# Kernel tuning notes

Measured on AMD Instinct MI355X. Metric: run time of the kernel, lower is better.

Reference implementation:

```python
import jax, jax.numpy as jnp
import numpy as np

ALPHA = 0.2          # LeakyReLU negative slope
NEG_INF = -9e15      # mask value from the torch code
B, N, F, E, H, S, T, L = 32, 128, 78, 12, 256, 20, 13, 3


def setup_inputs() -> dict:
    key = jax.random.key(0)
    ks = jax.random.split(key, 20)
    sc = 0.05  # param scale
    inp = {
        "node_features": jax.random.normal(ks[0], (B, N, F), jnp.float32),
        "edge_features": jax.random.normal(ks[1], (B, N, N, E), jnp.float32),
        "adj_matrix": jax.random.randint(ks[2], (B, N, N), 0, 2).astype(jnp.int32),
        "scaffold_features": jax.random.normal(ks[3], (B, S), jnp.float32),
        # node projection (Linear F->H, with bias)
        "W_node": jax.random.normal(ks[4], (F, H), jnp.float32) * sc,
        "b_node": jnp.zeros((H,), jnp.float32),
        # stacked GAT layer params: W (H->H, no bias), a (2H->1, no bias)
        "gat_W": jax.random.normal(ks[5], (L, H, H), jnp.float32) * sc,
        "gat_a": jax.random.normal(ks[6], (L, 2 * H), jnp.float32) * sc,
        # scaffold projection (S->H)
        "W_sc": jax.random.normal(ks[7], (S, H), jnp.float32) * sc,
        "b_sc": jnp.zeros((H,), jnp.float32),
        # graph_pooling MLP: H -> H/2 -> H/4 (shared for graph + scaffold paths)
        "gp_w1": jax.random.normal(ks[8], (H, H // 2), jnp.float32) * sc,
        "gp_b1": jnp.zeros((H // 2,), jnp.float32),
        "gp_w2": jax.random.normal(ks[9], (H // 2, H // 4), jnp.float32) * sc,
        "gp_b2": jnp.zeros((H // 4,), jnp.float32),
        # output MLP: (H/4 + H/4) -> H/2 -> T
        "out_w1": jax.random.normal(ks[10], (H // 2, H // 2), jnp.float32) * sc,
        "out_b1": jnp.zeros((H // 2,), jnp.float32),
        "out_w2": jax.random.normal(ks[11], (H // 2, T), jnp.float32) * sc,
        "out_b2": jnp.zeros((T,), jnp.float32),
    }
    return inp


def _gat_stack(x, adj_matrix, gat_W, gat_a):
    # x: (B,N,H); adj: (B,N,N) int
    mask = adj_matrix > 0
    n_layers, _, h_dim = gat_W.shape
    for l in range(n_layers):
        h = jnp.einsum("bnf,fh->bnh", x, gat_W[l])      # (B,N,H)
        a1, a2 = gat_a[l, :h_dim], gat_a[l, h_dim:]
        # a . [h_i ; h_j] == h_i.a1 + h_j.a2 (exact decomposition of the
        # O(N^2, 2H) concat in the torch code)
        s1 = h @ a1                                       # (B,N)
        s2 = h @ a2                                       # (B,N)
        e = jax.nn.leaky_relu(s1[:, :, None] + s2[:, None, :], ALPHA)
        att = jnp.where(mask, e, NEG_INF)                 # (B,N,N)
        att = jax.nn.softmax(att, axis=-1)
        h_prime = jnp.einsum("bij,bjh->bih", att, h)
        x = jax.nn.relu(h_prime)                          # relu after layer (dropout = identity, eval)
    return x


def _pool(z, gp_w1, gp_b1, gp_w2, gp_b2):
    z = jax.nn.relu(z @ gp_w1 + gp_b1)
    return jax.nn.relu(z @ gp_w2 + gp_b2)


def reference(node_features, edge_features, adj_matrix, scaffold_features,
              W_node, b_node, gat_W, gat_a, W_sc, b_sc,
              gp_w1, gp_b1, gp_w2, gp_b2, out_w1, out_b1, out_w2, out_b2):
    # edge_features is accepted but unused in the original forward
    x = node_features @ W_node + b_node                  # (B,N,H)
    x = _gat_stack(x, adj_matrix, gat_W, gat_a)
    graph = x.mean(axis=1)                               # (B,H)
    g = _pool(graph, gp_w1, gp_b1, gp_w2, gp_b2)         # (B,H/4)
    s = _pool(scaffold_features @ W_sc + b_sc, gp_w1, gp_b1, gp_w2, gp_b2)
    c = jnp.concatenate([g, s], axis=-1)                 # (B,H/2)
    hdn = jax.nn.relu(c @ out_w1 + out_b1)
    return hdn @ out_w2 + out_b2                         # (B,T)
```

## Files before the change

### kernel.cpp

```cpp
#include <hip/hip_runtime.h>
#include <hip/hip_bf16.h>

#define NEG_INF -9.0e15f

using u16 = unsigned short;

__device__ __forceinline__ float b2f(__hip_bfloat16 v) { return __bfloat162float(v); }
__device__ __forceinline__ float ldv(const float* p, int i) { return p[i]; }
__device__ __forceinline__ float ldv(const __hip_bfloat16* p, int i) { return __bfloat162float(p[i]); }

__device__ __forceinline__ void async16(const void* g, void* l) {
    __builtin_amdgcn_global_load_lds(
        (__attribute__((address_space(1))) void*)(g),
        (__attribute__((address_space(3))) void*)(l), 16, 0, 0);
}

__device__ __forceinline__ int sniff(const void* wnode) {
    const u16* w = (const u16*)wnode;
    int lane = threadIdx.x & 63;
    u16 u = w[2 * lane];
    int e = (u >> 7) & 0xFF;
    unsigned long long m = __ballot(e >= 100 && e <= 140);
    return __popcll(m) >= 48;
}

__global__ __launch_bounds__(256) void k_rep(
    const void* __restrict__ gat_W, const void* __restrict__ W_node,
    u16* __restrict__ Wrep, u16* __restrict__ Wnrep) {
    if (!sniff(W_node)) return;
    int b = blockIdx.x, t = threadIdx.x;
    if (b < 384) {
        int c = b / 48, idx = (b % 48) * 256 + t;
        ((uint4*)(Wrep + (size_t)c * 196608))[idx] = ((const uint4*)gat_W)[idx];
    } else {
        int bb = b - 384;
        int c = bb / 5, idx = (bb % 5) * 256 + t;
        if (idx < 1248)
            ((uint4*)(Wnrep + (size_t)c * 19968))[idx] = ((const uint4*)W_node)[idx];
    }
}

__global__ __launch_bounds__(256) void k_gat(
    const float* __restrict__ x, const void* __restrict__ gat_W,
    const u16* __restrict__ Wrep, const void* __restrict__ gat_a, int layer,
    const void* __restrict__ nf, const void* __restrict__ Wn_raw,
    const u16* __restrict__ Wnrep, const void* __restrict__ bn, int first,
    float* __restrict__ h, float* __restrict__ s1, float* __restrict__ s2) {
    __shared__ float xsT[256 * 10];
    const int t = threadIdx.x;
    const int bx = blockIdx.x;
    const int row0 = bx * 8;
    const int tx = t & 63, w = t >> 6;
    const int isbf = sniff(Wn_raw);
    const int c0 = 4 * tx;

    float acc0[4], acc1[4];

    if (isbf) {
        if (first) {
            const u16* nfu = (const u16*)nf;
            for (int i = t; i < 624; i += 256) {
                int r = i / 78, k = i - r * 78;
                xsT[k * 10 + r] = __uint_as_float(((unsigned)nfu[(row0 + r) * 78 + k]) << 16);
            }
            __syncthreads();
            const u16* Wnl = Wnrep + (size_t)(bx & 7) * 19968;
            const __hip_bfloat16* bnb = (const __hip_bfloat16*)bn;
            #pragma unroll
            for (int j = 0; j < 4; ++j) { acc0[j] = b2f(bnb[c0 + j]); acc1[j] = acc0[j]; }
            #pragma unroll 2
            for (int k = 0; k < 78; ++k) {
                uint2 wv = *(const uint2*)(Wnl + k * 256 + c0);
                float w0 = __uint_as_float(wv.x << 16);
                float w1 = __uint_as_float(wv.x & 0xffff0000u);
                float w2 = __uint_as_float(wv.y << 16);
                float w3 = __uint_as_float(wv.y & 0xffff0000u);
                float2 xp = *(const float2*)&xsT[k * 10 + 2 * w];
                acc0[0] += xp.x * w0; acc0[1] += xp.x * w1;
                acc0[2] += xp.x * w2; acc0[3] += xp.x * w3;
                acc1[0] += xp.y * w0; acc1[1] += xp.y * w1;
                acc1[2] += xp.y * w2; acc1[3] += xp.y * w3;
            }
            __syncthreads();
            #pragma unroll
            for (int j = 0; j < 4; ++j) {
                xsT[(c0 + j) * 10 + 2 * w]     = acc0[j];
                xsT[(c0 + j) * 10 + 2 * w + 1] = acc1[j];
            }
            __syncthreads();
        } else {
            int r = t >> 5, cb = (t & 31) * 8;
            const float4* xp = (const float4*)(x + (size_t)(row0 + r) * 256 + cb);
            float4 f0 = xp[0], f1 = xp[1];
            xsT[(cb + 0) * 10 + r] = f0.x; xsT[(cb + 1) * 10 + r] = f0.y;
            xsT[(cb + 2) * 10 + r] = f0.z; xsT[(cb + 3) * 10 + r] = f0.w;
            xsT[(cb + 4) * 10 + r] = f1.x; xsT[(cb + 5) * 10 + r] = f1.y;
            xsT[(cb + 6) * 10 + r] = f1.z; xsT[(cb + 7) * 10 + r] = f1.w;
            __syncthreads();
        }
        const u16* Wl = Wrep + (size_t)(bx & 7) * 196608 + (size_t)layer * 65536;
        #pragma unroll
        for (int j = 0; j < 4; ++j) { acc0[j] = 0.f; acc1[j] = 0.f; }
        #pragma unroll 4
        for (int k = 0; k < 256; ++k) {
            uint2 wv = *(const uint2*)(Wl + k * 256 + c0);
            float w0 = __uint_as_float(wv.x << 16);
            float w1 = __uint_as_float(wv.x & 0xffff0000u);
            float w2 = __uint_as_float(wv.y << 16);
            float w3 = __uint_as_float(wv.y & 0xffff0000u);
            float2 xp = *(const float2*)&xsT[k * 10 + 2 * w];
            acc0[0] += xp.x * w0; acc0[1] += xp.x * w1;
            acc0[2] += xp.x * w2; acc0[3] += xp.x * w3;
            acc1[0] += xp.y * w0; acc1[1] += xp.y * w1;
            acc1[2] += xp.y * w2; acc1[3] += xp.y * w3;
        }
        const __hip_bfloat16* ga = (const __hip_bfloat16*)gat_a + (size_t)layer * 512;
        float d10 = 0.f, d20 = 0.f, d11 = 0.f, d21 = 0.f;
        #pragma unroll
        for (int j = 0; j < 4; ++j) {
            float a1v = b2f(ga[c0 + j]), a2v = b2f(ga[256 + c0 + j]);
            d10 += acc0[j] * a1v; d20 += acc0[j] * a2v;
            d11 += acc1[j] * a1v; d21 += acc1[j] * a2v;
        }
        #pragma unroll
        for (int off = 1; off < 64; off <<= 1) {
            d10 += __shfl_xor(d10, off, 64); d20 += __shfl_xor(d20, off, 64);
            d11 += __shfl_xor(d11, off, 64); d21 += __shfl_xor(d21, off, 64);
        }
        if (tx == 0) {
            s1[row0 + 2 * w] = d10;     s2[row0 + 2 * w] = d20;
            s1[row0 + 2 * w + 1] = d11; s2[row0 + 2 * w + 1] = d21;
        }
        *(float4*)&h[(size_t)(row0 + 2 * w) * 256 + c0]     = (float4){acc0[0], acc0[1], acc0[2], acc0[3]};
        *(float4*)&h[(size_t)(row0 + 2 * w + 1) * 256 + c0] = (float4){acc1[0], acc1[1], acc1[2], acc1[3]};
    } else {
        const float* Wlf = (const float*)gat_W + (size_t)layer * 65536;
        const float* gaf = (const float*)gat_a + (size_t)layer * 512;
        if (first) {
            const float* nff = (const float*)nf;
            for (int i = t; i < 624; i += 256) {
                int r = i / 78, k = i - r * 78;
                xsT[k * 10 + r] = nff[(row0 + r) * 78 + k];
            }
            __syncthreads();
            const float* Wnf = (const float*)Wn_raw;
            const float* bnf = (const float*)bn;
            #pragma unroll
            for (int j = 0; j < 4; ++j) { acc0[j] = bnf[c0 + j]; acc1[j] = acc0[j]; }
            for (int k = 0; k < 78; ++k) {
                float4 wf = *(const float4*)(Wnf + k * 256 + c0);
                float2 xp = *(const float2*)&xsT[k * 10 + 2 * w];
                acc0[0] += xp.x * wf.x; acc0[1] += xp.x * wf.y;
                acc0[2] += xp.x * wf.z; acc0[3] += xp.x * wf.w;
                acc1[0] += xp.y * wf.x; acc1[1] += xp.y * wf.y;
                acc1[2] += xp.y * wf.z; acc1[3] += xp.y * wf.w;
            }
            __syncthreads();
            #pragma unroll
            for (int j = 0; j < 4; ++j) {
                xsT[(c0 + j) * 10 + 2 * w]     = acc0[j];
                xsT[(c0 + j) * 10 + 2 * w + 1] = acc1[j];
            }
            __syncthreads();
        } else {
            int r = t >> 5, cb = (t & 31) * 8;
            const float4* xp = (const float4*)(x + (size_t)(row0 + r) * 256 + cb);
            float4 f0 = xp[0], f1 = xp[1];
            xsT[(cb + 0) * 10 + r] = f0.x; xsT[(cb + 1) * 10 + r] = f0.y;
            xsT[(cb + 2) * 10 + r] = f0.z; xsT[(cb + 3) * 10 + r] = f0.w;
            xsT[(cb + 4) * 10 + r] = f1.x; xsT[(cb + 5) * 10 + r] = f1.y;
            xsT[(cb + 6) * 10 + r] = f1.z; xsT[(cb + 7) * 10 + r] = f1.w;
            __syncthreads();
        }
        #pragma unroll
        for (int j = 0; j < 4; ++j) { acc0[j] = 0.f; acc1[j] = 0.f; }
        #pragma unroll 4
        for (int k = 0; k < 256; ++k) {
            float4 wf = *(const float4*)(Wlf + k * 256 + c0);
            float2 xp = *(const float2*)&xsT[k * 10 + 2 * w];
            acc0[0] += xp.x * wf.x; acc0[1] += xp.x * wf.y;
            acc0[2] += xp.x * wf.z; acc0[3] += xp.x * wf.w;
            acc1[0] += xp.y * wf.x; acc1[1] += xp.y * wf.y;
            acc1[2] += xp.y * wf.z; acc1[3] += xp.y * wf.w;
        }
        float d10 = 0.f, d20 = 0.f, d11 = 0.f, d21 = 0.f;
        #pragma unroll
        for (int j = 0; j < 4; ++j) {
            float a1v = gaf[c0 + j], a2v = gaf[256 + c0 + j];
            d10 += acc0[j] * a1v; d20 += acc0[j] * a2v;
            d11 += acc1[j] * a1v; d21 += acc1[j] * a2v;
        }
        #pragma unroll
        for (int off = 1; off < 64; off <<= 1) {
            d10 += __shfl_xor(d10, off, 64); d20 += __shfl_xor(d20, off, 64);
            d11 += __shfl_xor(d11, off, 64); d21 += __shfl_xor(d21, off, 64);
        }
        if (tx == 0) {
            s1[row0 + 2 * w] = d10;     s2[row0 + 2 * w] = d20;
            s1[row0 + 2 * w + 1] = d11; s2[row0 + 2 * w + 1] = d21;
        }
        *(float4*)&h[(size_t)(row0 + 2 * w) * 256 + c0]     = (float4){acc0[0], acc0[1], acc0[2], acc0[3]};
        *(float4*)&h[(size_t)(row0 + 2 * w + 1) * 256 + c0] = (float4){acc1[0], acc1[1], acc1[2], acc1[3]};
    }
}

__global__ __launch_bounds__(256) void k_attn(
    const float* __restrict__ h, const float* __restrict__ s1,
    const float* __restrict__ s2, const int* __restrict__ adj,
    float* __restrict__ x, float* __restrict__ gpart, int do_pool) {
    __shared__ float att_t[128][10];
    __shared__ __align__(16) float hbuf[2][32 * 256];
    __shared__ float pool_red[4][256];
    int blk = blockIdx.x, b = blk >> 4, i0 = (blk & 15) << 3;
    int t = threadIdx.x, w = t >> 6, lane = t & 63;
    const char* hbytes = (const char*)(h + (size_t)b * 32768);
    const int ph = blk & 3;
    {
        char* lb = (char*)&hbuf[0][0];
        const char* g = hbytes + ph * 32768;
        #pragma unroll
        for (int i = 0; i < 8; ++i)
            async16(g + i * 4096 + t * 16, lb + i * 4096 + t * 16);
    }
    {
        int cc0 = lane, cc1 = lane + 64;
        int ir0 = i0 + 2 * w, ir1 = ir0 + 1;
        const int* a0 = adj + (size_t)(b * 128 + ir0) * 128;
        const int* a1 = adj + (size_t)(b * 128 + ir1) * 128;
        int m00 = a0[cc0], m01 = a0[cc1], m10 = a1[cc0], m11 = a1[cc1];
        float sv0 = s1[b * 128 + ir0], sv1 = s1[b * 128 + ir1];
        float t0 = s2[b * 128 + cc0],  t1 = s2[b * 128 + cc1];
        float e00 = sv0 + t0; e00 = (e00 >= 0.f) ? e00 : 0.2f * e00;
        float e01 = sv0 + t1; e01 = (e01 >= 0.f) ? e01 : 0.2f * e01;
        float e10 = sv1 + t0; e10 = (e10 >= 0.f) ? e10 : 0.2f * e10;
        float e11 = sv1 + t1; e11 = (e11 >= 0.f) ? e11 : 0.2f * e11;
        float v00 = (m00 > 0) ? e00 : NEG_INF;
        float v01 = (m01 > 0) ? e01 : NEG_INF;
        float v10 = (m10 > 0) ? e10 : NEG_INF;
        float v11 = (m11 > 0) ? e11 : NEG_INF;
        float mx0 = fmaxf(v00, v01), mx1 = fmaxf(v10, v11);
        #pragma unroll
        for (int off = 1; off < 64; off <<= 1) {
            mx0 = fmaxf(mx0, __shfl_xor(mx0, off, 64));
            mx1 = fmaxf(mx1, __shfl_xor(mx1, off, 64));
        }
        float p00 = __expf(v00 - mx0), p01 = __expf(v01 - mx0);
        float p10 = __expf(v10 - mx1), p11 = __expf(v11 - mx1);
        float s0 = p00 + p01, ss1 = p10 + p11;
        #pragma unroll
        for (int off = 1; off < 64; off <<= 1) {
            s0  += __shfl_xor(s0, off, 64);
            ss1 += __shfl_xor(ss1, off, 64);
        }
        float inv0 = 1.0f / s0, inv1 = 1.0f / ss1;
        att_t[cc0][2 * w]     = p00 * inv0;
        att_t[cc1][2 * w]     = p01 * inv0;
        att_t[cc0][2 * w + 1] = p10 * inv1;
        att_t[cc1][2 * w + 1] = p11 * inv1;
    }
    __syncthreads();
    int tx = t & 63, ty = t >> 6;
    float acc0[4] = {0.f, 0.f, 0.f, 0.f}, acc1[4] = {0.f, 0.f, 0.f, 0.f};
    for (int c = 0; c < 4; ++c) {
        if (c < 3) {
            char* lb = (char*)&hbuf[(c + 1) & 1][0];
            const char* g = hbytes + (((c + 1 + ph) & 3) * 32768);
            #pragma unroll
            for (int i = 0; i < 8; ++i)
                async16(g + i * 4096 + t * 16, lb + i * 4096 + t * 16);
        }
        const float* hc = &hbuf[c & 1][0];
        const int jb = ((c + ph) & 3) * 32;
        #pragma unroll 4
        for (int jj = 0; jj < 32; ++jj) {
            float4 hv = *(const float4*)&hc[jj * 256 + 4 * tx];
            float2 ap = *(const float2*)&att_t[jb + jj][2 * ty];
            acc0[0] += ap.x * hv.x; acc0[1] += ap.x * hv.y;
            acc0[2] += ap.x * hv.z; acc0[3] += ap.x * hv.w;
            acc1[0] += ap.y * hv.x; acc1[1] += ap.y * hv.y;
            acc1[2] += ap.y * hv.z; acc1[3] += ap.y * hv.w;
        }
        __syncthreads();
    }
    if (!do_pool) {
        float4 o0 = {fmaxf(acc0[0],0.f), fmaxf(acc0[1],0.f), fmaxf(acc0[2],0.f), fmaxf(acc0[3],0.f)};
        float4 o1 = {fmaxf(acc1[0],0.f), fmaxf(acc1[1],0.f), fmaxf(acc1[2],0.f), fmaxf(acc1[3],0.f)};
        *(float4*)&x[(size_t)(b * 128 + i0 + 2 * ty)     * 256 + 4 * tx] = o0;
        *(float4*)&x[(size_t)(b * 128 + i0 + 2 * ty + 1) * 256 + 4 * tx] = o1;
    } else {
        float4 pr = {(fmaxf(acc0[0],0.f) + fmaxf(acc1[0],0.f)) * (1.f/128.f),
                     (fmaxf(acc0[1],0.f) + fmaxf(acc1[1],0.f)) * (1.f/128.f),
                     (fmaxf(acc0[2],0.f) + fmaxf(acc1[2],0.f)) * (1.f/128.f),
                     (fmaxf(acc0[3],0.f) + fmaxf(acc1[3],0.f)) * (1.f/128.f)};
        *(float4*)&pool_red[ty][4 * tx] = pr;
        __syncthreads();
        if (t < 64) {
            float4 r0 = ((const float4*)&pool_red[0][0])[t];
            float4 r1 = ((const float4*)&pool_red[1][0])[t];
            float4 r2 = ((const float4*)&pool_red[2][0])[t];
            float4 r3 = ((const float4*)&pool_red[3][0])[t];
            float4 o = {r0.x+r1.x+r2.x+r3.x, r0.y+r1.y+r2.y+r3.y,
                        r0.z+r1.z+r2.z+r3.z, r0.w+r1.w+r2.w+r3.w};
            *(float4*)&gpart[((size_t)b * 16 + (blk & 15)) * 256 + 4 * t] = o;
        }
    }
}

template <typename T>
__device__ __forceinline__ void head_body(
    int b, int t, const float* __restrict__ gpart,
    const T* scaf, const T* W_sc, const T* b_sc,
    const T* gp_w1, const T* gp_b1, const T* gp_w2, const T* gp_b2,
    const T* out_w1, const T* out_b1, const T* out_w2, const T* out_b2,
    float* gin_s, float* sproj, float* scaf_s,
    float* red1, float* red2, float* z1g, float* z1s,
    float* cvec, float* hdn, float* outv) {
    float g = 0.f;
    #pragma unroll
    for (int gg = 0; gg < 16; ++gg) g += gpart[((size_t)b * 16 + gg) * 256 + t];
    gin_s[t] = g;
    if (t < 20) scaf_s[t] = ldv(scaf, b * 20 + t);
    __syncthreads();
    {
        float sa = ldv(b_sc, t);
        #pragma unroll
        for (int k = 0; k < 20; ++k) sa += scaf_s[k] * ldv(W_sc, k * 256 + t);
        sproj[t] = sa;
    }
    __syncthreads();
    {
        int j = t & 127, khalf = t >> 7;
        int k0 = khalf * 128;
        float a1 = 0.f, a2 = 0.f;
        #pragma unroll 16
        for (int kk = 0; kk < 128; ++kk) {
            int k = k0 + kk;
            float wv = ldv(gp_w1, k * 128 + j);
            a1 += gin_s[k] * wv;
            a2 += sproj[k] * wv;
        }
        red1[t] = a1; red2[t] = a2;
    }
    __syncthreads();
    if (t < 128) {
        float bb = ldv(gp_b1, t);
        z1g[t] = fmaxf(bb + red1[t] + red1[t + 128], 0.f);
        z1s[t] = fmaxf(bb + red2[t] + red2[t + 128], 0.f);
    }
    __syncthreads();
    {
        int j = t & 63, q = t >> 6;
        int k0 = q * 32;
        float a1 = 0.f, a2 = 0.f;
        #pragma unroll
        for (int kk = 0; kk < 32; ++kk) {
            int k = k0 + kk;
            float wv = ldv(gp_w2, k * 64 + j);
            a1 += z1g[k] * wv;
            a2 += z1s[k] * wv;
        }
        red1[t] = a1; red2[t] = a2;
    }
    __syncthreads();
    if (t < 64) {
        float bb = ldv(gp_b2, t);
        cvec[t]      = fmaxf(bb + red1[t] + red1[t + 64] + red1[t + 128] + red1[t + 192], 0.f);
        cvec[64 + t] = fmaxf(bb + red2[t] + red2[t + 64] + red2[t + 128] + red2[t + 192], 0.f);
    }
    __syncthreads();
    {
        int j = t & 127, khalf = t >> 7;
        int k0 = khalf * 64;
        float a = 0.f;
        #pragma unroll 16
        for (int kk = 0; kk < 64; ++kk) {
            int k = k0 + kk;
            a += cvec[k] * ldv(out_w1, k * 128 + j);
        }
        red1[t] = a;
    }
    __syncthreads();
    if (t < 128) hdn[t] = fmaxf(ldv(out_b1, t) + red1[t] + red1[t + 128], 0.f);
    __syncthreads();
    if (t < 13) {
        float a = ldv(out_b2, t);
        #pragma unroll 16
        for (int k = 0; k < 128; ++k) a += hdn[k] * ldv(out_w2, k * 13 + t);
        outv[t] = a;
    }
}

__global__ __launch_bounds__(256) void k_head(
    const float* __restrict__ gpart, const void* __restrict__ scaf,
    const void* __restrict__ W_sc, const void* __restrict__ b_sc,
    const void* __restrict__ gp_w1, const void* __restrict__ gp_b1,
    const void* __restrict__ gp_w2, const void* __restrict__ gp_b2,
    const void* __restrict__ out_w1, const void* __restrict__ out_b1,
    const void* __restrict__ out_w2, const void* __restrict__ out_b2,
    void* __restrict__ out, const void* __restrict__ Wn) {
    int isbf = sniff(Wn);
    int b = blockIdx.x;
    int t = threadIdx.x;
    __shared__ float gin_s[256], sproj[256], scaf_s[20];
    __shared__ float red1[256], red2[256];
    __shared__ float z1g[128], z1s[128], cvec[128], hdn[128], outv[13];
    if (isbf) {
        head_body<__hip_bfloat16>(b, t, gpart,
            (const __hip_bfloat16*)scaf, (const __hip_bfloat16*)W_sc, (const __hip_bfloat16*)b_sc,
            (const __hip_bfloat16*)gp_w1, (const __hip_bfloat16*)gp_b1,
            (const __hip_bfloat16*)gp_w2, (const __hip_bfloat16*)gp_b2,
            (const __hip_bfloat16*)out_w1, (const __hip_bfloat16*)out_b1,
            (const __hip_bfloat16*)out_w2, (const __hip_bfloat16*)out_b2,
            gin_s, sproj, scaf_s, red1, red2, z1g, z1s, cvec, hdn, outv);
    } else {
        head_body<float>(b, t, gpart,
            (const float*)scaf, (const float*)W_sc, (const float*)b_sc,
            (const float*)gp_w1, (const float*)gp_b1,
            (const float*)gp_w2, (const float*)gp_b2,
            (const float*)out_w1, (const float*)out_b1,
            (const float*)out_w2, (const float*)out_b2,
            gin_s, sproj, scaf_s, red1, red2, z1g, z1s, cvec, hdn, outv);
    }
    __syncthreads();
    if (t < 13) {
        if (isbf) ((__hip_bfloat16*)out)[b * 13 + t] = __float2bfloat16(outv[t]);
        else      ((float*)out)[b * 13 + t] = outv[t];
    }
}

extern "C" void kernel_launch(void* const* d_in, const int* in_sizes, int n_in,
                              void* d_out, int out_size, void* d_ws, size_t ws_size,
                              hipStream_t stream) {
    (void)in_sizes; (void)n_in; (void)out_size; (void)ws_size;
    const void* nf     = d_in[0];
    const int*  adj    = (const int*)d_in[2];
    const void* scaf   = d_in[3];
    const void* W_node = d_in[4];
    const void* b_node = d_in[5];
    const void* gat_W  = d_in[6];
    const void* gat_a  = d_in[7];
    const void* W_sc   = d_in[8];
    const void* b_sc   = d_in[9];
    const void* gp_w1  = d_in[10];
    const void* gp_b1  = d_in[11];
    const void* gp_w2  = d_in[12];
    const void* gp_b2  = d_in[13];
    const void* out_w1 = d_in[14];
    const void* out_b1 = d_in[15];
    const void* out_w2 = d_in[16];
    const void* out_b2 = d_in[17];

    float* ws    = (float*)d_ws;
    float* x     = ws;
    float* h     = ws + 1048576;
    float* s1    = ws + 2097152;
    float* s2    = s1 + 4096;
    float* gpart = s2 + 4096;
    u16*   Wrep  = (u16*)(gpart + 131072);
    u16*   Wnrep = Wrep + 8 * 196608;

    k_rep<<<424, 256, 0, stream>>>(gat_W, W_node, Wrep, Wnrep);
    for (int l = 0; l < 3; ++l) {
        k_gat<<<512, 256, 0, stream>>>(x, gat_W, Wrep, gat_a, l,
                                       nf, W_node, Wnrep, b_node, (l == 0) ? 1 : 0,
                                       h, s1, s2);
        k_attn<<<512, 256, 0, stream>>>(h, s1, s2, adj, x, gpart, (l == 2) ? 1 : 0);
    }
    k_head<<<32, 256, 0, stream>>>(gpart, scaf, W_sc, b_sc, gp_w1, gp_b1, gp_w2, gp_b2,
                                   out_w1, out_b1, out_w2, out_b2, d_out, W_node);
}
```

Measured before the change: 227.2 us.

## Drop weight replication kernel and halve rows per GAT projection block

Removes the k_rep kernel that copied gat_W and W_node into eight per-XCD replicas, so k_gat now reads the original weights directly. Each k_gat block now handles 4 rows (one per wave) instead of 8, and the grid doubles to 1024 blocks. The x tile is stored untransposed in shared memory. This saves one launch and the replication traffic and adds parallelism, at the cost of halving weight reuse per block and possible L2 contention across XCDs on the shared weights.

```diff
diff --git a/kernel.cpp b/kernel.cpp
--- a/kernel.cpp
+++ b/kernel.cpp
@@ -8,6 +8,7 @@
 __device__ __forceinline__ float b2f(__hip_bfloat16 v) { return __bfloat162float(v); }
 __device__ __forceinline__ float ldv(const float* p, int i) { return p[i]; }
 __device__ __forceinline__ float ldv(const __hip_bfloat16* p, int i) { return __bfloat162float(p[i]); }
+__device__ __forceinline__ float bu2f(u16 u) { return __uint_as_float(((unsigned)u) << 16); }
 
 __device__ __forceinline__ void async16(const void* g, void* l) {
     __builtin_amdgcn_global_load_lds(
@@ -24,50 +25,31 @@
     return __popcll(m) >= 48;
 }
 
-__global__ __launch_bounds__(256) void k_rep(
-    const void* __restrict__ gat_W, const void* __restrict__ W_node,
-    u16* __restrict__ Wrep, u16* __restrict__ Wnrep) {
-    if (!sniff(W_node)) return;
-    int b = blockIdx.x, t = threadIdx.x;
-    if (b < 384) {
-        int c = b / 48, idx = (b % 48) * 256 + t;
-        ((uint4*)(Wrep + (size_t)c * 196608))[idx] = ((const uint4*)gat_W)[idx];
-    } else {
-        int bb = b - 384;
-        int c = bb / 5, idx = (bb % 5) * 256 + t;
-        if (idx < 1248)
-            ((uint4*)(Wnrep + (size_t)c * 19968))[idx] = ((const uint4*)W_node)[idx];
-    }
-}
-
 __global__ __launch_bounds__(256) void k_gat(
     const float* __restrict__ x, const void* __restrict__ gat_W,
-    const u16* __restrict__ Wrep, const void* __restrict__ gat_a, int layer,
+    const void* __restrict__ gat_a, int layer,
     const void* __restrict__ nf, const void* __restrict__ Wn_raw,
-    const u16* __restrict__ Wnrep, const void* __restrict__ bn, int first,
+    const void* __restrict__ bn, int first,
     float* __restrict__ h, float* __restrict__ s1, float* __restrict__ s2) {
-    __shared__ float xsT[256 * 10];
-    const int t = threadIdx.x;
-    const int bx = blockIdx.x;
-    const int row0 = bx * 8;
-    const int tx = t & 63, w = t >> 6;
+    __shared__ float xs[4][256];
+    const int t = threadIdx.x, bx = blockIdx.x;
+    const int row0 = bx * 4;
+    const int w = t >> 6, tx = t & 63, c0 = 4 * tx;
     const int isbf = sniff(Wn_raw);
-    const int c0 = 4 * tx;
-
-    float acc0[4], acc1[4];
+    float acc[4];
 
     if (isbf) {
         if (first) {
             const u16* nfu = (const u16*)nf;
-            for (int i = t; i < 624; i += 256) {
+            for (int i = t; i < 312; i += 256) {
                 int r = i / 78, k = i - r * 78;
-                xsT[k * 10 + r] = __uint_as_float(((unsigned)nfu[(row0 + r) * 78 + k]) << 16);
+                xs[r][k] = bu2f(nfu[(row0 + r) * 78 + k]);
             }
             __syncthreads();
-            const u16* Wnl = Wnrep + (size_t)(bx & 7) * 19968;
+            const u16* Wnl = (const u16*)Wn_raw;
             const __hip_bfloat16* bnb = (const __hip_bfloat16*)bn;
             #pragma unroll
-            for (int j = 0; j < 4; ++j) { acc0[j] = b2f(bnb[c0 + j]); acc1[j] = acc0[j]; }
+            for (int j = 0; j < 4; ++j) acc[j] = b2f(bnb[c0 + j]);
             #pragma unroll 2
             for (int k = 0; k < 78; ++k) {
                 uint2 wv = *(const uint2*)(Wnl + k * 256 + c0);
@@ -75,32 +57,21 @@
                 float w1 = __uint_as_float(wv.x & 0xffff0000u);
                 float w2 = __uint_as_float(wv.y << 16);
                 float w3 = __uint_as_float(wv.y & 0xffff0000u);
-                float2 xp = *(const float2*)&xsT[k * 10 + 2 * w];
-                acc0[0] += xp.x * w0; acc0[1] += xp.x * w1;
-                acc0[2] += xp.x * w2; acc0[3] += xp.x * w3;
-                acc1[0] += xp.y * w0; acc1[1] += xp.y * w1;
-                acc1[2] += xp.y * w2; acc1[3] += xp.y * w3;
+                float xv = xs[w][k];
+                acc[0] += xv * w0; acc[1] += xv * w1;
+                acc[2] += xv * w2; acc[3] += xv * w3;
             }
             __syncthreads();
-            #pragma unroll
-            for (int j = 0; j < 4; ++j) {
-                xsT[(c0 + j) * 10 + 2 * w]     = acc0[j];
-                xsT[(c0 + j) * 10 + 2 * w + 1] = acc1[j];
-            }
+            *(float4*)&xs[w][c0] = (float4){acc[0], acc[1], acc[2], acc[3]};
             __syncthreads();
         } else {
-            int r = t >> 5, cb = (t & 31) * 8;
-            const float4* xp = (const float4*)(x + (size_t)(row0 + r) * 256 + cb);
-            float4 f0 = xp[0], f1 = xp[1];
-            xsT[(cb + 0) * 10 + r] = f0.x; xsT[(cb + 1) * 10 + r] = f0.y;
-            xsT[(cb + 2) * 10 + r] = f0.z; xsT[(cb + 3) * 10 + r] = f0.w;
-            xsT[(cb + 4) * 10 + r] = f1.x; xsT[(cb + 5) * 10 + r] = f1.y;
-            xsT[(cb + 6) * 10 + r] = f1.z; xsT[(cb + 7) * 10 + r] = f1.w;
-            __syncthreads();
-        }
-        const u16* Wl = Wrep + (size_t)(bx & 7) * 196608 + (size_t)layer * 65536;
-        #pragma unroll
-        for (int j = 0; j < 4; ++j) { acc0[j] = 0.f; acc1[j] = 0.f; }
+            int r = t >> 6, pos = t & 63;
+            ((float4*)&xs[r][0])[pos] = ((const float4*)&x[(size_t)(row0 + r) * 256])[pos];
+            __syncthreads();
+        }
+        const u16* Wl = (const u16*)gat_W + (size_t)layer * 65536;
+        #pragma unroll
+        for (int j = 0; j < 4; ++j) acc[j] = 0.f;
         #pragma unroll 4
         for (int k = 0; k < 256; ++k) {
             uint2 wv = *(const uint2*)(Wl + k * 256 + c0);
@@ -108,99 +79,74 @@
             float w1 = __uint_as_float(wv.x & 0xffff0000u);
             float w2 = __uint_as_float(wv.y << 16);
             float w3 = __uint_as_float(wv.y & 0xffff0000u);
-            float2 xp = *(const float2*)&xsT[k * 10 + 2 * w];
-            acc0[0] += xp.x * w0; acc0[1] += xp.x * w1;
-            acc0[2] += xp.x * w2; acc0[3] += xp.x * w3;
-            acc1[0] += xp.y * w0; acc1[1] += xp.y * w1;
-            acc1[2] += xp.y * w2; acc1[3] += xp.y * w3;
+            float xv = xs[w][k];
+            acc[0] += xv * w0; acc[1] += xv * w1;
+            acc[2] += xv * w2; acc[3] += xv * w3;
         }
         const __hip_bfloat16* ga = (const __hip_bfloat16*)gat_a + (size_t)layer * 512;
-        float d10 = 0.f, d20 = 0.f, d11 = 0.f, d21 = 0.f;
+        float d1 = 0.f, d2 = 0.f;
         #pragma unroll
         for (int j = 0; j < 4; ++j) {
-            float a1v = b2f(ga[c0 + j]), a2v = b2f(ga[256 + c0 + j]);
-            d10 += acc0[j] * a1v; d20 += acc0[j] * a2v;
-            d11 += acc1[j] * a1v; d21 += acc1[j] * a2v;
+            d1 += acc[j] * b2f(ga[c0 + j]);
+            d2 += acc[j] * b2f(ga[256 + c0 + j]);
         }
         #pragma unroll
         for (int off = 1; off < 64; off <<= 1) {
-            d10 += __shfl_xor(d10, off, 64); d20 += __shfl_xor(d20, off, 64);
-            d11 += __shfl_xor(d11, off, 64); d21 += __shfl_xor(d21, off, 64);
-        }
-        if (tx == 0) {
-            s1[row0 + 2 * w] = d10;     s2[row0 + 2 * w] = d20;
-            s1[row0 + 2 * w + 1] = d11; s2[row0 + 2 * w + 1] = d21;
-        }
-        *(float4*)&h[(size_t)(row0 + 2 * w) * 256 + c0]     = (float4){acc0[0], acc0[1], acc0[2], acc0[3]};
-        *(float4*)&h[(size_t)(row0 + 2 * w + 1) * 256 + c0] = (float4){acc1[0], acc1[1], acc1[2], acc1[3]};
+            d1 += __shfl_xor(d1, off, 64);
+            d2 += __shfl_xor(d2, off, 64);
+        }
+        if (tx == 0) { s1[row0 + w] = d1; s2[row0 + w] = d2; }
+        *(float4*)&h[(size_t)(row0 + w) * 256 + c0] = (float4){acc[0], acc[1], acc[2], acc[3]};
     } else {
         const float* Wlf = (const float*)gat_W + (size_t)layer * 65536;
         const float* gaf = (const float*)gat_a + (size_t)layer * 512;
         if (first) {
             const float* nff = (const float*)nf;
-            for (int i = t; i < 624; i += 256) {
+            for (int i = t; i < 312; i += 256) {
                 int r = i / 78, k = i - r * 78;
-                xsT[k * 10 + r] = nff[(row0 + r) * 78 + k];
+                xs[r][k] = nff[(row0 + r) * 78 + k];
             }
             __syncthreads();
             const float* Wnf = (const float*)Wn_raw;
             const float* bnf = (const float*)bn;
             #pragma unroll
-            for (int j = 0; j < 4; ++j) { acc0[j] = bnf[c0 + j]; acc1[j] = acc0[j]; }
+            for (int j = 0; j < 4; ++j) acc[j] = bnf[c0 + j];
             for (int k = 0; k < 78; ++k) {
                 float4 wf = *(const float4*)(Wnf + k * 256 + c0);
-                float2 xp = *(const float2*)&xsT[k * 10 + 2 * w];
-                acc0[0] += xp.x * wf.x; acc0[1] += xp.x * wf.y;
-                acc0[2] += xp.x * wf.z; acc0[3] += xp.x * wf.w;
-                acc1[0] += xp.y * wf.x; acc1[1] += xp.y * wf.y;
-                acc1[2] += xp.y * wf.z; acc1[3] += xp.y * wf.w;
+                float xv = xs[w][k];
+                acc[0] += xv * wf.x; acc[1] += xv * wf.y;
+                acc[2] += xv * wf.z; acc[3] += xv * wf.w;
             }
             __syncthreads();
-            #pragma unroll
-            for (int j = 0; j < 4; ++j) {
-                xsT[(c0 + j) * 10 + 2 * w]     = acc0[j];
-                xsT[(c0 + j) * 10 + 2 * w + 1] = acc1[j];
-            }
+            *(float4*)&xs[w][c0] = (float4){acc[0], acc[1], acc[2], acc[3]};
             __syncthreads();
         } else {
-            int r = t >> 5, cb = (t & 31) * 8;
-            const float4* xp = (const float4*)(x + (size_t)(row0 + r) * 256 + cb);
-            float4 f0 = xp[0], f1 = xp[1];
-            xsT[(cb + 0) * 10 + r] = f0.x; xsT[(cb + 1) * 10 + r] = f0.y;
-            xsT[(cb + 2) * 10 + r] = f0.z; xsT[(cb + 3) * 10 + r] = f0.w;
-            xsT[(cb + 4) * 10 + r] = f1.x; xsT[(cb + 5) * 10 + r] = f1.y;
-            xsT[(cb + 6) * 10 + r] = f1.z; xsT[(cb + 7) * 10 + r] = f1.w;
-            __syncthreads();
-        }
-        #pragma unroll
-        for (int j = 0; j < 4; ++j) { acc0[j] = 0.f; acc1[j] = 0.f; }
+            int r = t >> 6, pos = t & 63;
+            ((float4*)&xs[r][0])[pos] = ((const float4*)&x[(size_t)(row0 + r) * 256])[pos];
+            __syncthreads();
+        }
+        #pragma unroll
+        for (int j = 0; j < 4; ++j) acc[j] = 0.f;
         #pragma unroll 4
         for (int k = 0; k < 256; ++k) {
             float4 wf = *(const float4*)(Wlf + k * 256 + c0);
-            float2 xp = *(const float2*)&xsT[k * 10 + 2 * w];
-            acc0[0] += xp.x * wf.x; acc0[1] += xp.x * wf.y;
-            acc0[2] += xp.x * wf.z; acc0[3] += xp.x * wf.w;
-            acc1[0] += xp.y * wf.x; acc1[1] += xp.y * wf.y;
-            acc1[2] += xp.y * wf.z; acc1[3] += xp.y * wf.w;
-        }
-        float d10 = 0.f, d20 = 0.f, d11 = 0.f, d21 = 0.f;
+            float xv = xs[w][k];
+            acc[0] += xv * wf.x; acc[1] += xv * wf.y;
+            acc[2] += xv * wf.z; acc[3] += xv * wf.w;
+        }
+        float d1 = 0.f, d2 = 0.f;
         #pragma unroll
         for (int j = 0; j < 4; ++j) {
-            float a1v = gaf[c0 + j], a2v = gaf[256 + c0 + j];
-            d10 += acc0[j] * a1v; d20 += acc0[j] * a2v;
-            d11 += acc1[j] * a1v; d21 += acc1[j] * a2v;
+            d1 += acc[j] * gaf[c0 + j];
+            d2 += acc[j] * gaf[256 + c0 + j];
         }
         #pragma unroll
         for (int off = 1; off < 64; off <<= 1) {
-            d10 += __shfl_xor(d10, off, 64); d20 += __shfl_xor(d20, off, 64);
-            d11 += __shfl_xor(d11, off, 64); d21 += __shfl_xor(d21, off, 64);
-        }
-        if (tx == 0) {
-            s1[row0 + 2 * w] = d10;     s2[row0 + 2 * w] = d20;
-            s1[row0 + 2 * w + 1] = d11; s2[row0 + 2 * w + 1] = d21;
-        }
-        *(float4*)&h[(size_t)(row0 + 2 * w) * 256 + c0]     = (float4){acc0[0], acc0[1], acc0[2], acc0[3]};
-        *(float4*)&h[(size_t)(row0 + 2 * w + 1) * 256 + c0] = (float4){acc1[0], acc1[1], acc1[2], acc1[3]};
+            d1 += __shfl_xor(d1, off, 64);
+            d2 += __shfl_xor(d2, off, 64);
+        }
+        if (tx == 0) { s1[row0 + w] = d1; s2[row0 + w] = d2; }
+        *(float4*)&h[(size_t)(row0 + w) * 256 + c0] = (float4){acc[0], acc[1], acc[2], acc[3]};
     }
 }
 
@@ -456,14 +402,11 @@
     float* s1    = ws + 2097152;
     float* s2    = s1 + 4096;
     float* gpart = s2 + 4096;
-    u16*   Wrep  = (u16*)(gpart + 131072);
-    u16*   Wnrep = Wrep + 8 * 196608;
-
-    k_rep<<<424, 256, 0, stream>>>(gat_W, W_node, Wrep, Wnrep);
+
     for (int l = 0; l < 3; ++l) {
-        k_gat<<<512, 256, 0, stream>>>(x, gat_W, Wrep, gat_a, l,
-                                       nf, W_node, Wnrep, b_node, (l == 0) ? 1 : 0,
-                                       h, s1, s2);
+        k_gat<<<1024, 256, 0, stream>>>(x, gat_W, gat_a, l,
+                                        nf, W_node, b_node, (l == 0) ? 1 : 0,
+                                        h, s1, s2);
         k_attn<<<512, 256, 0, stream>>>(h, s1, s2, adj, x, gpart, (l == 2) ? 1 : 0);
     }
     k_head<<<32, 256, 0, stream>>>(gpart, scaf, W_sc, b_sc, gp_w1, gp_b1, gp_w2, gp_b2,
```

Measured after the change: 256.8 us. 13.1% more time.
